# Kernel optimization log

Measured on AMD Instinct MI355X. Metric: run time of the kernel, lower is better.

The kernel has to match this reference:

```python
import jax, jax.numpy as jnp
import numpy as np

ALPHA = 0.25
GAMMA = 2.0
EPS = 1e-4


def calc_iou(a, b):
    # a: [A,4] anchors xyxy, b: [M,4] gt boxes xyxy -> [A,M]
    area = (b[:, 2] - b[:, 0]) * (b[:, 3] - b[:, 1])  # [M]
    iw = jnp.minimum(a[:, 2:3], b[None, :, 2]) - jnp.maximum(a[:, 0:1], b[None, :, 0])
    ih = jnp.minimum(a[:, 3:4], b[None, :, 3]) - jnp.maximum(a[:, 1:2], b[None, :, 1])
    iw = jnp.clip(iw, 0.0)
    ih = jnp.clip(ih, 0.0)
    anchor_area = ((a[:, 2] - a[:, 0]) * (a[:, 3] - a[:, 1]))[:, None]
    ua = jnp.clip(anchor_area + area[None, :] - iw * ih, 1e-8)
    return iw * ih / ua


def setup_inputs() -> dict:
    B, A, K, M = 8, 120000, 80, 32
    key = jax.random.key(0)
    k1, k2, k3, k4, k5, k6, k7 = jax.random.split(key, 7)
    classifications = jax.random.uniform(k1, (B, A, K), dtype=jnp.float32)
    regressions = jax.random.normal(k2, (B, A, 4), dtype=jnp.float32) * 0.1
    # anchors: valid xyxy boxes with positive width/height
    a_xy = jax.random.uniform(k3, (A, 2), minval=0.0, maxval=480.0)
    a_wh = jax.random.uniform(k4, (A, 2), minval=16.0, maxval=128.0)
    anchors = jnp.concatenate([a_xy, a_xy + a_wh], axis=1)[None].astype(jnp.float32)
    # annotations: [B, M, 5] valid gt boxes, labels in [0, K)
    g_xy = jax.random.uniform(k5, (B, M, 2), minval=0.0, maxval=400.0)
    g_wh = jax.random.uniform(k6, (B, M, 2), minval=20.0, maxval=120.0)
    labels = jax.random.randint(k7, (B, M, 1), 0, K).astype(jnp.float32)
    annotations = jnp.concatenate([g_xy, g_xy + g_wh, labels], axis=2).astype(jnp.float32)
    return {"classifications": classifications, "regressions": regressions,
            "anchors": anchors, "annotations": annotations}


def reference(classifications, regressions, anchors, annotations):
    anchor = anchors[0]  # [A,4]
    aw = anchor[:, 2] - anchor[:, 0]
    ah = anchor[:, 3] - anchor[:, 1]
    acx = anchor[:, 0] + 0.5 * aw
    acy = anchor[:, 1] + 0.5 * ah
    reg_scale = jnp.array([0.1, 0.1, 0.2, 0.2], dtype=classifications.dtype)

    def per_item(cls, reg, ann):
        # cls: [A,K], reg: [A,4], ann: [M,5]
        valid = ann[:, 4] != -1.0  # [M] padding mask
        c = jnp.clip(cls, EPS, 1.0 - EPS)
        iou = jnp.where(valid[None, :], calc_iou(anchor, ann[:, :4]), -1.0)  # [A,M]
        iou_max = iou.max(axis=1)
        iou_argmax = iou.argmax(axis=1)
        assigned = ann[iou_argmax]  # [A,5] gather
        pos = iou_max >= 0.5
        neg = iou_max < 0.4
        num_pos = pos.sum().astype(c.dtype)
        # targets: 1 at assigned class for positives, 0 for negatives, -1 = ignore
        onehot = jax.nn.one_hot(assigned[:, 4].astype(jnp.int32), c.shape[1], dtype=c.dtype)
        t = jnp.where(pos[:, None], onehot, jnp.where(neg[:, None], 0.0, -1.0))
        alpha_factor = jnp.where(t == 1.0, ALPHA, 1.0 - ALPHA)
        focal_weight = jnp.where(t == 1.0, 1.0 - c, c)
        bce = -(t * jnp.log(c) + (1.0 - t) * jnp.log(1.0 - c))
        cls_loss = jnp.where(t != -1.0, alpha_factor * focal_weight ** GAMMA * bce, 0.0)
        cls_loss = cls_loss.sum() / jnp.maximum(num_pos, 1.0)
        gw0 = assigned[:, 2] - assigned[:, 0]
        gh0 = assigned[:, 3] - assigned[:, 1]
        gcx = assigned[:, 0] + 0.5 * gw0
        gcy = assigned[:, 1] + 0.5 * gh0
        gw = jnp.maximum(gw0, 1.0)
        gh = jnp.maximum(gh0, 1.0)
        rt = jnp.stack([(gcx - acx) / aw, (gcy - acy) / ah,
                        jnp.log(gw / aw), jnp.log(gh / ah)], axis=1) / reg_scale
        diff = jnp.abs(rt - reg)
        smooth = jnp.where(diff <= 1.0 / 9.0, 0.5 * 9.0 * diff ** 2, diff - 0.5 / 9.0)
        reg_loss = jnp.where(num_pos > 0.0,
                             (smooth * pos[:, None]).sum() / jnp.maximum(num_pos * 4.0, 1.0),
                             0.0)
        return cls_loss, reg_loss

    cls_l, reg_l = jax.vmap(per_item)(classifications, regressions, annotations)
    return cls_l.mean(keepdims=True), reg_l.mean(keepdims=True)
```

## Files before the change

kernel.cpp:

```cpp
#include <hip/hip_runtime.h>

#define NB 8
#define NA 120000
#define NK 80
#define NM 32

#define ALPHA_F 0.25f
#define EPS_F 1e-4f

#define BLK 256
#define BPB ((NA + BLK - 1) / BLK)

__device__ __forceinline__ float clampc(float x) {
    return fminf(fmaxf(x, EPS_F), 1.0f - EPS_F);
}
__device__ __forceinline__ float negl(float c) {
    return (1.0f - ALPHA_F) * c * c * (-__logf(1.0f - c));
}
__device__ __forceinline__ float posl(float c) {
    const float omc = 1.0f - c;
    return ALPHA_F * omc * omc * (-__logf(c));
}
__device__ __forceinline__ float negl4(float4 v) {
    return negl(clampc(v.x)) + negl(clampc(v.y)) + negl(clampc(v.z)) + negl(clampc(v.w));
}

__global__ __launch_bounds__(BLK) void fused_kernel(
    const float* __restrict__ anchors,
    const float* __restrict__ regressions,
    const float* __restrict__ annotations,
    const float* __restrict__ cls,
    float* __restrict__ part)
{
    const int b = blockIdx.x / BPB;
    const int blk = blockIdx.x % BPB;
    const int a0 = blk * BLK;
    const int a = a0 + threadIdx.x;

    __shared__ float ann[NM * 5];
    __shared__ float barea[NM];
    __shared__ int s_st[BLK];
    if (threadIdx.x < NM * 5) ann[threadIdx.x] = annotations[b * NM * 5 + threadIdx.x];
    __syncthreads();
    if (threadIdx.x < NM) {
        const float* r = &ann[threadIdx.x * 5];
        barea[threadIdx.x] = (r[2] - r[0]) * (r[3] - r[1]);
    }
    __syncthreads();

    float reg_local = 0.0f;
    float pos_local = 0.0f;
    float cls_local = 0.0f;

    int st = -2;
    if (a < NA) {
        const float4 av = ((const float4*)anchors)[a];
        const float aw = av.z - av.x;
        const float ah = av.w - av.y;
        const float aarea = aw * ah;

        float bi = -1.0f, bu = 1.0f;
        int bm = 0;
        #pragma unroll
        for (int m = 0; m < NM; ++m) {
            const float bx1 = ann[m * 5 + 0];
            const float by1 = ann[m * 5 + 1];
            const float bx2 = ann[m * 5 + 2];
            const float by2 = ann[m * 5 + 3];
            const float lbl = ann[m * 5 + 4];
            const float iw = fmaxf(fminf(av.z, bx2) - fmaxf(av.x, bx1), 0.0f);
            const float ih = fmaxf(fminf(av.w, by2) - fmaxf(av.y, by1), 0.0f);
            float inter = iw * ih;
            float ua = fmaxf(aarea + barea[m] - inter, 1e-8f);
            if (lbl == -1.0f) { inter = -1.0f; ua = 1.0f; }
            if (m == 0 || inter * bu > bi * ua) { bi = inter; bu = ua; bm = m; }
        }

        if (bi >= 0.5f * bu) {
            st = (int)ann[bm * 5 + 4];
            const float bx1 = ann[bm * 5 + 0];
            const float by1 = ann[bm * 5 + 1];
            const float bx2 = ann[bm * 5 + 2];
            const float by2 = ann[bm * 5 + 3];
            const float gw0 = bx2 - bx1;
            const float gh0 = by2 - by1;
            const float gcx = bx1 + 0.5f * gw0;
            const float gcy = by1 + 0.5f * gh0;
            const float gw = fmaxf(gw0, 1.0f);
            const float gh = fmaxf(gh0, 1.0f);
            const float acx = av.x + 0.5f * aw;
            const float acy = av.y + 0.5f * ah;
            const float rt0 = ((gcx - acx) / aw) / 0.1f;
            const float rt1 = ((gcy - acy) / ah) / 0.1f;
            const float rt2 = logf(gw / aw) / 0.2f;
            const float rt3 = logf(gh / ah) / 0.2f;
            const float4 rg = ((const float4*)regressions)[b * NA + a];
            float s = 0.0f, d;
            d = fabsf(rt0 - rg.x); s += (d <= 1.0f / 9.0f) ? 4.5f * d * d : d - 0.5f / 9.0f;
            d = fabsf(rt1 - rg.y); s += (d <= 1.0f / 9.0f) ? 4.5f * d * d : d - 0.5f / 9.0f;
            d = fabsf(rt2 - rg.z); s += (d <= 1.0f / 9.0f) ? 4.5f * d * d : d - 0.5f / 9.0f;
            d = fabsf(rt3 - rg.w); s += (d <= 1.0f / 9.0f) ? 4.5f * d * d : d - 0.5f / 9.0f;
            reg_local = s;
            pos_local = 1.0f;
        } else if (bi >= 0.4f * bu) {
            st = -1;
        }
    }
    s_st[threadIdx.x] = st;
    __syncthreads();

    const float4* __restrict__ p = (const float4*)(cls + ((size_t)b * NA + a0) * NK);
    const int n_rows = (a0 + BLK <= NA) ? BLK : (NA - a0);

    if (n_rows == BLK) {
        #pragma unroll
        for (int o = 0; o < 4; ++o) {
            float4 v[5];
            #pragma unroll
            for (int u = 0; u < 5; ++u)
                v[u] = p[(o * 5 + u) * BLK + threadIdx.x];
            #pragma unroll
            for (int u = 0; u < 5; ++u) {
                const int idx = (o * 5 + u) * BLK + threadIdx.x;
                const int row = idx / 20;
                const int k0 = (idx - row * 20) * 4;
                const int s = s_st[row];
                const float m = (s == -1) ? 0.0f : 1.0f;
                float l = m * negl4(v[u]);
                if (s >= k0 && s < k0 + 4) {
                    const float c = clampc((s == k0) ? v[u].x : (s == k0 + 1) ? v[u].y
                                         : (s == k0 + 2) ? v[u].z : v[u].w);
                    l += posl(c) - negl(c);
                }
                cls_local += l;
            }
        }
    } else {
        const int n4 = n_rows * 20;
        for (int idx = threadIdx.x; idx < n4; idx += BLK) {
            const float4 v = p[idx];
            const int row = idx / 20;
            const int k0 = (idx - row * 20) * 4;
            const int s = s_st[row];
            const float m = (s == -1) ? 0.0f : 1.0f;
            float l = m * negl4(v);
            if (s >= k0 && s < k0 + 4) {
                const float c = clampc((s == k0) ? v.x : (s == k0 + 1) ? v.y
                                     : (s == k0 + 2) ? v.z : v.w);
                l += posl(c) - negl(c);
            }
            cls_local += l;
        }
    }

    #pragma unroll
    for (int o = 32; o > 0; o >>= 1) {
        cls_local += __shfl_down(cls_local, o, 64);
        reg_local += __shfl_down(reg_local, o, 64);
        pos_local += __shfl_down(pos_local, o, 64);
    }
    __shared__ float wc[BLK / 64], wr[BLK / 64], wp[BLK / 64];
    const int lane = threadIdx.x & 63;
    const int wid = threadIdx.x >> 6;
    if (lane == 0) { wc[wid] = cls_local; wr[wid] = reg_local; wp[wid] = pos_local; }
    __syncthreads();
    if (threadIdx.x == 0) {
        float csum = 0.0f, rsum = 0.0f, psum = 0.0f;
        #pragma unroll
        for (int i = 0; i < BLK / 64; ++i) { csum += wc[i]; rsum += wr[i]; psum += wp[i]; }
        float* q = &part[(size_t)blockIdx.x * 3];
        q[0] = csum; q[1] = rsum; q[2] = psum;
    }
}

__global__ __launch_bounds__(256) void finalize_kernel(
    const float* __restrict__ part,
    float* __restrict__ out)
{
    __shared__ float red[3][4];
    float cs_total = 0.0f, rs_total = 0.0f;
    for (int b = 0; b < NB; ++b) {
        float c = 0.0f, r = 0.0f, p = 0.0f;
        for (int i = threadIdx.x; i < BPB; i += 256) {
            const float* q = &part[(size_t)(b * BPB + i) * 3];
            c += q[0]; r += q[1]; p += q[2];
        }
        #pragma unroll
        for (int o = 32; o > 0; o >>= 1) {
            c += __shfl_down(c, o, 64);
            r += __shfl_down(r, o, 64);
            p += __shfl_down(p, o, 64);
        }
        const int lane = threadIdx.x & 63;
        const int wid = threadIdx.x >> 6;
        if (lane == 0) { red[0][wid] = c; red[1][wid] = r; red[2][wid] = p; }
        __syncthreads();
        if (threadIdx.x == 0) {
            const float C = red[0][0] + red[0][1] + red[0][2] + red[0][3];
            const float R = red[1][0] + red[1][1] + red[1][2] + red[1][3];
            const float P = red[2][0] + red[2][1] + red[2][2] + red[2][3];
            cs_total += C / fmaxf(P, 1.0f);
            rs_total += (P > 0.0f) ? R / fmaxf(P * 4.0f, 1.0f) : 0.0f;
        }
        __syncthreads();
    }
    if (threadIdx.x == 0) {
        out[0] = cs_total / (float)NB;
        out[1] = rs_total / (float)NB;
    }
}

extern "C" void kernel_launch(void* const* d_in, const int* in_sizes, int n_in,
                              void* d_out, int out_size, void* d_ws, size_t ws_size,
                              hipStream_t stream) {
    const float* cls = (const float*)d_in[0];
    const float* reg = (const float*)d_in[1];
    const float* anc = (const float*)d_in[2];
    const float* ann = (const float*)d_in[3];

    float* part = (float*)d_ws;
    float* out = (float*)d_out;

    fused_kernel<<<NB * BPB, BLK, 0, stream>>>(anc, reg, ann, cls, part);
    finalize_kernel<<<1, 256, 0, stream>>>(part, out);
}
```

Baseline: 83.93 us.

## Compute dense negative focal loss, correct positives and ignored anchors separately

The streaming classification pass now sums the negative-class focal term over every element unconditionally, with no per-row state lookup, integer division or compare. Positive anchors add a per-anchor correction from a single scalar load of the target class. Ignored anchors are collected into a shared list and their negative contribution is re-read and subtracted afterward. Partial sums are stored as float4 for vectorized writes and reads. This trims ALU work in the hot loop but adds a shared atomic, a second read of ignored rows, and subtraction-based cancellation that can slightly change float rounding.

Result: no change. 83.54 us (-0.5%).

```diff
diff --git a/kernel.cpp b/kernel.cpp
--- a/kernel.cpp
+++ b/kernel.cpp
@@ -39,7 +39,9 @@
 
     __shared__ float ann[NM * 5];
     __shared__ float barea[NM];
-    __shared__ int s_st[BLK];
+    __shared__ int s_ign[BLK];
+    __shared__ int s_nign;
+    if (threadIdx.x == 0) s_nign = 0;
     if (threadIdx.x < NM * 5) ann[threadIdx.x] = annotations[b * NM * 5 + threadIdx.x];
     __syncthreads();
     if (threadIdx.x < NM) {
@@ -52,7 +54,6 @@
     float pos_local = 0.0f;
     float cls_local = 0.0f;
 
-    int st = -2;
     if (a < NA) {
         const float4 av = ((const float4*)anchors)[a];
         const float aw = av.z - av.x;
@@ -77,7 +78,7 @@
         }
 
         if (bi >= 0.5f * bu) {
-            st = (int)ann[bm * 5 + 4];
+            const int st = (int)ann[bm * 5 + 4];
             const float bx1 = ann[bm * 5 + 0];
             const float by1 = ann[bm * 5 + 1];
             const float bx2 = ann[bm * 5 + 2];
@@ -102,11 +103,13 @@
             d = fabsf(rt3 - rg.w); s += (d <= 1.0f / 9.0f) ? 4.5f * d * d : d - 0.5f / 9.0f;
             reg_local = s;
             pos_local = 1.0f;
+            const float c = clampc(cls[((size_t)b * NA + a) * NK + st]);
+            cls_local = posl(c) - negl(c);
         } else if (bi >= 0.4f * bu) {
-            st = -1;
-        }
-    }
-    s_st[threadIdx.x] = st;
+            const int k = atomicAdd(&s_nign, 1);
+            s_ign[k] = threadIdx.x;
+        }
+    }
     __syncthreads();
 
     const float4* __restrict__ p = (const float4*)(cls + ((size_t)b * NA + a0) * NK);
@@ -120,36 +123,23 @@
             for (int u = 0; u < 5; ++u)
                 v[u] = p[(o * 5 + u) * BLK + threadIdx.x];
             #pragma unroll
-            for (int u = 0; u < 5; ++u) {
-                const int idx = (o * 5 + u) * BLK + threadIdx.x;
-                const int row = idx / 20;
-                const int k0 = (idx - row * 20) * 4;
-                const int s = s_st[row];
-                const float m = (s == -1) ? 0.0f : 1.0f;
-                float l = m * negl4(v[u]);
-                if (s >= k0 && s < k0 + 4) {
-                    const float c = clampc((s == k0) ? v[u].x : (s == k0 + 1) ? v[u].y
-                                         : (s == k0 + 2) ? v[u].z : v[u].w);
-                    l += posl(c) - negl(c);
-                }
-                cls_local += l;
-            }
+            for (int u = 0; u < 5; ++u)
+                cls_local += negl4(v[u]);
         }
     } else {
         const int n4 = n_rows * 20;
-        for (int idx = threadIdx.x; idx < n4; idx += BLK) {
-            const float4 v = p[idx];
-            const int row = idx / 20;
-            const int k0 = (idx - row * 20) * 4;
-            const int s = s_st[row];
-            const float m = (s == -1) ? 0.0f : 1.0f;
-            float l = m * negl4(v);
-            if (s >= k0 && s < k0 + 4) {
-                const float c = clampc((s == k0) ? v.x : (s == k0 + 1) ? v.y
-                                     : (s == k0 + 2) ? v.z : v.w);
-                l += posl(c) - negl(c);
-            }
-            cls_local += l;
+        for (int idx = threadIdx.x; idx < n4; idx += BLK)
+            cls_local += negl4(p[idx]);
+    }
+
+    const int nign = s_nign;
+    if (nign > 0) {
+        const int total = nign * 20;
+        for (int i = threadIdx.x; i < total; i += BLK) {
+            const int e = i / 20;
+            const int f = i - e * 20;
+            const int r = s_ign[e];
+            cls_local -= negl4(p[r * 20 + f]);
         }
     }
 
@@ -168,8 +158,9 @@
         float csum = 0.0f, rsum = 0.0f, psum = 0.0f;
         #pragma unroll
         for (int i = 0; i < BLK / 64; ++i) { csum += wc[i]; rsum += wr[i]; psum += wp[i]; }
-        float* q = &part[(size_t)blockIdx.x * 3];
-        q[0] = csum; q[1] = rsum; q[2] = psum;
+        float4 q;
+        q.x = csum; q.y = rsum; q.z = psum; q.w = 0.0f;
+        ((float4*)part)[blockIdx.x] = q;
     }
 }
 
@@ -182,8 +173,8 @@
     for (int b = 0; b < NB; ++b) {
         float c = 0.0f, r = 0.0f, p = 0.0f;
         for (int i = threadIdx.x; i < BPB; i += 256) {
-            const float* q = &part[(size_t)(b * BPB + i) * 3];
-            c += q[0]; r += q[1]; p += q[2];
+            const float4 q = ((const float4*)part)[b * BPB + i];
+            c += q.x; r += q.y; p += q.z;
         }
         #pragma unroll
         for (int o = 32; o > 0; o >>= 1) {
```
